# Kernel optimization log

Hardware: AMD Instinct MI355X
Metric: run time of the kernel (lower is better)

## Reference

```python
import jax, jax.numpy as jnp
import numpy as np

HIDDEN = 1024
INTER = 1408
N_EXPERTS = 8
TOP_K = 2
BATCH, SEQ = 2, 1024


def setup_inputs() -> dict:
    key = jax.random.key(0)
    k1, k2, k3, k4, k5 = jax.random.split(key, 5)
    scale_in = 1.0 / np.sqrt(HIDDEN)
    scale_mid = 1.0 / np.sqrt(INTER)
    return {
        "hidden_states": jax.random.normal(k1, (BATCH, SEQ, HIDDEN), dtype=jnp.float32),
        # router: torch Linear(hidden, n_experts, bias=False) -> weight [E, hidden]
        "router_w": jax.random.normal(k2, (N_EXPERTS, HIDDEN), dtype=jnp.float32) * scale_in,
        # per-expert SwiGLU MLP weights, stored pre-transposed for x @ W
        "wg": jax.random.normal(k3, (N_EXPERTS, HIDDEN, INTER), dtype=jnp.float32) * scale_in,
        "wu": jax.random.normal(k4, (N_EXPERTS, HIDDEN, INTER), dtype=jnp.float32) * scale_in,
        "wd": jax.random.normal(k5, (N_EXPERTS, INTER, HIDDEN), dtype=jnp.float32) * scale_mid,
    }


def reference(hidden_states, router_w, wg, wu, wd):
    B, S, D = hidden_states.shape
    x = hidden_states.reshape(-1, D)  # [T, D]
    T = x.shape[0]
    E = router_w.shape[0]

    # Router: softmax over experts in float32, then top-k and renormalize (norm_topk_prob=True)
    logits = x @ router_w.T  # [T, E]
    probs = jax.nn.softmax(logits.astype(jnp.float32), axis=-1)
    topk_w, topk_idx = jax.lax.top_k(probs, TOP_K)  # [T, K]
    topk_w = topk_w / jnp.sum(topk_w, axis=-1, keepdims=True)
    topk_w = topk_w.astype(x.dtype)

    # Dense combine weights [T, E]: zero for unrouted experts -> math-identical to sparse dispatch
    combine = jnp.zeros((T, E), dtype=x.dtype).at[
        jnp.arange(T)[:, None], topk_idx
    ].add(topk_w)

    # Expert SwiGLU MLPs computed as batched GEMMs over experts
    g = jnp.einsum('td,edf->etf', x, wg)  # [E, T, INTER]
    u = jnp.einsum('td,edf->etf', x, wu)
    h = jax.nn.silu(g) * u
    y = jnp.einsum('etf,efd->etd', h, wd)  # [E, T, D]

    out = jnp.einsum('etd,te->td', y, combine)  # weighted combine
    return out.reshape(B, S, D)
```

## Files before the change

kernel.cpp:

```cpp
#include <hip/hip_runtime.h>
#include <math.h>

#define HIDDEN 1024
#define INTER  1408
#define NEXP   8
#define NTOK   2048
#define KSPLIT_LEN 704

typedef short s16x8 __attribute__((ext_vector_type(8)));
typedef float f32x4 __attribute__((ext_vector_type(4)));

static __device__ __forceinline__ short f2b(float f) {
  union { float f; unsigned u; } v; v.f = f;
  unsigned u = v.u;
  unsigned r = (u + 0x7FFFu + ((u >> 16) & 1u)) >> 16;
  return (short)r;
}

__global__ __launch_bounds__(256) void router_choice(
    const float* __restrict__ x, const float* __restrict__ rw,
    int* __restrict__ ce, float2* __restrict__ cw)
{
  int wave = threadIdx.x >> 6;
  int lane = threadIdx.x & 63;
  int t = blockIdx.x * 4 + wave;
  if (t >= NTOK) return;
  const float* xt = x + (size_t)t * HIDDEN;
  float xr[16];
#pragma unroll
  for (int i = 0; i < 16; ++i) xr[i] = xt[lane + 64 * i];
  float logits[NEXP];
#pragma unroll
  for (int e = 0; e < NEXP; ++e) {
    const float* w = rw + e * HIDDEN;
    float acc = 0.f;
#pragma unroll
    for (int i = 0; i < 16; ++i) acc = fmaf(xr[i], w[lane + 64 * i], acc);
#pragma unroll
    for (int off = 32; off > 0; off >>= 1) acc += __shfl_xor(acc, off);
    logits[e] = acc;
  }
  if (lane == 0) {
    float mx = logits[0];
#pragma unroll
    for (int e = 1; e < NEXP; ++e) mx = fmaxf(mx, logits[e]);
    float p[NEXP];
#pragma unroll
    for (int e = 0; e < NEXP; ++e) p[e] = expf(logits[e] - mx);
    int i0 = 0;
#pragma unroll
    for (int e = 1; e < NEXP; ++e) if (p[e] > p[i0]) i0 = e;
    int i1 = (i0 == 0) ? 1 : 0;
#pragma unroll
    for (int e = 0; e < NEXP; ++e) { if (e != i0 && p[e] > p[i1]) i1 = e; }
    float denom = p[i0] + p[i1];
    ce[t] = i0 | (i1 << 8);
    cw[t] = make_float2(p[i0] / denom, p[i1] / denom);
  }
}

__global__ __launch_bounds__(256) void build_lists(
    const int* __restrict__ ce, const float2* __restrict__ cw,
    int* __restrict__ counts, int* __restrict__ base,
    int* __restrict__ tok_list, float* __restrict__ w_list)
{
  int e = blockIdx.x;
  int tid = threadIdx.x;
  __shared__ int hall[256][8];
  __shared__ int hsum[8];
  __shared__ int scan[256];

  int cloc[8];
  int h[8] = {0,0,0,0,0,0,0,0};
  int myc = 0;
#pragma unroll
  for (int j = 0; j < 8; ++j) {
    int c = ce[tid * 8 + j];
    cloc[j] = c;
    int e0 = c & 255, e1 = (c >> 8) & 255;
    h[e0]++; h[e1]++;
    myc += (e0 == e) + (e1 == e);
  }
#pragma unroll
  for (int k = 0; k < 8; ++k) hall[tid][k] = h[k];
  scan[tid] = myc;
  __syncthreads();

  if (tid < 8) {
    int s = 0;
    for (int i = 0; i < 256; ++i) s += hall[i][tid];
    hsum[tid] = s;
  }
  int v = myc;
  for (int off = 1; off < 256; off <<= 1) {
    int prev = (tid >= off) ? scan[tid - off] : 0;
    __syncthreads();
    v = v + prev;
    scan[tid] = v;
    __syncthreads();
  }
  int pos = v - myc;

  if (tid == 0) {
    int b = 0;
    for (int k = 0; k < e; ++k) b += hsum[k];
    base[e] = b;
    counts[e] = hsum[e];
  }

#pragma unroll
  for (int j = 0; j < 8; ++j) {
    int t = tid * 8 + j;
    int c = cloc[j];
    int e0 = c & 255, e1 = (c >> 8) & 255;
    if (e0 == e) {
      float2 w = cw[t];
      tok_list[e * NTOK + pos] = t;
      w_list[e * NTOK + pos] = w.x;
      pos++;
    } else if (e1 == e) {
      float2 w = cw[t];
      tok_list[e * NTOK + pos] = t | (1 << 16);
      w_list[e * NTOK + pos] = w.y;
      pos++;
    }
  }
}

static __device__ __forceinline__ void tconv_tile(
    const float* __restrict__ ie, short* __restrict__ oe,
    int K, int N, int k0, int n0, int tid, float (*t)[65])
{
  int c4 = (tid & 15) * 4, r = tid >> 4;
#pragma unroll
  for (int p = 0; p < 4; ++p) {
    float4 v = *(const float4*)(ie + (size_t)(k0 + r + p * 16) * N + n0 + c4);
    t[r + p * 16][c4 + 0] = v.x;
    t[r + p * 16][c4 + 1] = v.y;
    t[r + p * 16][c4 + 2] = v.z;
    t[r + p * 16][c4 + 3] = v.w;
  }
  __syncthreads();
  int rn = tid >> 2, ck = (tid & 3) * 16;
  s16x8 o0, o1;
#pragma unroll
  for (int j = 0; j < 8; ++j) o0[j] = f2b(t[ck + j][rn]);
#pragma unroll
  for (int j = 0; j < 8; ++j) o1[j] = f2b(t[ck + 8 + j][rn]);
  short* op = oe + (size_t)(n0 + rn) * K + k0 + ck;
  *(s16x8*)(op) = o0;
  *(s16x8*)(op + 8) = o1;
}

__global__ __launch_bounds__(256) void prep_kernel(
    const float* __restrict__ x, const float* __restrict__ wg,
    const float* __restrict__ wu, const float* __restrict__ wd,
    short* __restrict__ xb, short* __restrict__ wgT,
    short* __restrict__ wuT, short* __restrict__ wdT)
{
  __shared__ float t[64][65];
  int id = blockIdx.x;
  int tid = threadIdx.x;
  if (id < 1024) {
    size_t i = (size_t)id * 256 + tid;
    const float4* p = (const float4*)x;
    float4 a = p[2 * i], b = p[2 * i + 1];
    s16x8 o;
    o[0] = f2b(a.x); o[1] = f2b(a.y); o[2] = f2b(a.z); o[3] = f2b(a.w);
    o[4] = f2b(b.x); o[5] = f2b(b.y); o[6] = f2b(b.z); o[7] = f2b(b.w);
    *(s16x8*)(xb + 8 * i) = o;
    return;
  }
  int id2 = id - 1024;
  int seg = id2 / 2816;
  int r = id2 - seg * 2816;
  int e = r / 352;
  int rem = r - e * 352;
  if (seg < 2) {
    int kt = rem / 22, nt = rem - kt * 22;
    const float* ie = (seg == 0 ? wg : wu) + (size_t)e * HIDDEN * INTER;
    short* oe = (seg == 0 ? wgT : wuT) + (size_t)e * HIDDEN * INTER;
    tconv_tile(ie, oe, HIDDEN, INTER, kt * 64, nt * 64, tid, t);
  } else {
    int kt = rem >> 4, nt = rem & 15;
    const float* ie = wd + (size_t)e * HIDDEN * INTER;
    short* oe = wdT + (size_t)e * HIDDEN * INTER;
    tconv_tile(ie, oe, INTER, HIDDEN, kt * 64, nt * 64, tid, t);
  }
}


__global__ __launch_bounds__(256, 2) void gateup_mfma(
    const short* __restrict__ xb, const short* __restrict__ wgT,
    const short* __restrict__ wuT,
    const int* __restrict__ counts, const int* __restrict__ base,
    const int* __restrict__ tok_list, short* __restrict__ hbuf)
{
  int id = blockIdx.x;
  int xcd = id & 7;
  int rest = id >> 3;
  int mslot = rest & 15;
  int g = (rest >> 4) * 8 + xcd;
  int e = g / 11;
  int n0 = (g - e * 11) * 128;
  int cnt = counts[e];
  int m0 = mslot * 128;
  if (m0 >= cnt) return;

  __shared__ short As[128 * 32];
  __shared__ short Bg[128 * 32];
  __shared__ short Bu[128 * 32];
  __shared__ int toks[128];

  int tid = threadIdx.x;
  if (tid < 128) {
    int r = m0 + tid;
    toks[tid] = tok_list[e * NTOK + (r < cnt ? r : cnt - 1)] & 0xFFFF;
  }
  __syncthreads();

  int sr = tid >> 1;
  int h = tid & 1;
  int key = (sr >> 1) & 3;
  int pair = ((2 * h) ^ key) >> 1;
  int sw = (key & 1) * 8;
  const short* gA = xb + (size_t)toks[sr] * HIDDEN + pair * 16;
  const short* gG = wgT + ((size_t)e * INTER + n0 + sr) * HIDDEN + pair * 16;
  const short* gU = wuT + ((size_t)e * INTER + n0 + sr) * HIDDEN + pair * 16;
  short* wA0 = &As[sr * 32 + h * 16 + sw];
  short* wA1 = &As[sr * 32 + h * 16 + (8 - sw)];
  short* wG0 = &Bg[sr * 32 + h * 16 + sw];
  short* wG1 = &Bg[sr * 32 + h * 16 + (8 - sw)];
  short* wU0 = &Bu[sr * 32 + h * 16 + sw];
  short* wU1 = &Bu[sr * 32 + h * 16 + (8 - sw)];

  int wv = tid >> 6, lane = tid & 63;
  int wm = wv & 1, wn = wv >> 1;
  int q = lane >> 4, ml = lane & 15;
  int chk = q ^ ((ml >> 1) & 3);
  const short* ard = &As[(wm * 64 + ml) * 32 + chk * 8];
  const short* grd = &Bg[(wn * 64 + ml) * 32 + chk * 8];
  const short* urd = &Bu[(wn * 64 + ml) * 32 + chk * 8];

  f32x4 accg[4][4], accu[4][4];
#pragma unroll
  for (int i = 0; i < 4; ++i)
#pragma unroll
    for (int j = 0; j < 4; ++j) { accg[i][j] = (f32x4)0.f; accu[i][j] = (f32x4)0.f; }

  s16x8 a0 = *(const s16x8*)(gA);     s16x8 a1 = *(const s16x8*)(gA + 8);
  s16x8 g0 = *(const s16x8*)(gG);     s16x8 g1 = *(const s16x8*)(gG + 8);
  s16x8 u0 = *(const s16x8*)(gU);     s16x8 u1 = *(const s16x8*)(gU + 8);

  for (int k0 = 0; k0 < HIDDEN; k0 += 32) {
    __syncthreads();
    *(s16x8*)wA0 = a0; *(s16x8*)wA1 = a1;
    *(s16x8*)wG0 = g0; *(s16x8*)wG1 = g1;
    *(s16x8*)wU0 = u0; *(s16x8*)wU1 = u1;
    __syncthreads();

    int kn = (k0 + 32) & (HIDDEN - 1);
    a0 = *(const s16x8*)(gA + kn);     a1 = *(const s16x8*)(gA + kn + 8);
    g0 = *(const s16x8*)(gG + kn);     g1 = *(const s16x8*)(gG + kn + 8);
    u0 = *(const s16x8*)(gU + kn);     u1 = *(const s16x8*)(gU + kn + 8);

    s16x8 af[4], gf[4], uf[4];
#pragma unroll
    for (int i = 0; i < 4; ++i) af[i] = *(const s16x8*)(ard + i * 16 * 32);
#pragma unroll
    for (int j = 0; j < 4; ++j) {
      gf[j] = *(const s16x8*)(grd + j * 16 * 32);
      uf[j] = *(const s16x8*)(urd + j * 16 * 32);
    }
#pragma unroll
    for (int i = 0; i < 4; ++i)
#pragma unroll
      for (int j = 0; j < 4; ++j) {
        accg[i][j] = __builtin_amdgcn_mfma_f32_16x16x32_bf16(af[i], gf[j], accg[i][j], 0, 0, 0);
        accu[i][j] = __builtin_amdgcn_mfma_f32_16x16x32_bf16(af[i], uf[j], accu[i][j], 0, 0, 0);
      }
  }

  int hb = base[e];
#pragma unroll
  for (int i = 0; i < 4; ++i)
#pragma unroll
    for (int ii = 0; ii < 4; ++ii) {
      int r = m0 + wm * 64 + i * 16 + q * 4 + ii;
      if (r < cnt) {
        short* hp = hbuf + (size_t)(hb + r) * INTER + n0 + wn * 64 + ml;
#pragma unroll
        for (int j = 0; j < 4; ++j) {
          float gg = accg[i][j][ii], uu = accu[i][j][ii];
          float hh = (gg / (1.f + __expf(-gg))) * uu;
          hp[j * 16] = f2b(hh);
        }
      }
    }
}

__global__ __launch_bounds__(256, 3) void down_mfma(
    const short* __restrict__ hbuf, const short* __restrict__ wdT,
    const int* __restrict__ counts, const int* __restrict__ base,
    const int* __restrict__ tok_list, const float* __restrict__ w_list,
    float* __restrict__ ybuf)
{
  int id = blockIdx.x;
  int xcd = id & 7;
  int rest = id >> 3;
  int mslot = rest & 15;
  int g = (rest >> 4) * 8 + xcd;
  int e = g >> 4;
  int ks = (g >> 3) & 1;
  int n0 = (g & 7) * 128;
  int cnt = counts[e];
  int m0 = mslot * 128;
  if (m0 >= cnt) return;

  __shared__ short As[128 * 32];
  __shared__ short Bs[128 * 32];

  int tid = threadIdx.x;
  int hb = base[e];
  int kbeg = ks * KSPLIT_LEN, kend = kbeg + KSPLIT_LEN;

  int sr = tid >> 1;
  int h = tid & 1;
  int key = (sr >> 1) & 3;
  int pair = ((2 * h) ^ key) >> 1;
  int sw = (key & 1) * 8;
  int ra = m0 + sr; if (ra >= cnt) ra = cnt - 1;
  const short* gA = hbuf + (size_t)(hb + ra) * INTER + pair * 16;
  const short* gB = wdT + ((size_t)e * HIDDEN + n0 + sr) * INTER + pair * 16;
  short* wA0 = &As[sr * 32 + h * 16 + sw];
  short* wA1 = &As[sr * 32 + h * 16 + (8 - sw)];
  short* wB0 = &Bs[sr * 32 + h * 16 + sw];
  short* wB1 = &Bs[sr * 32 + h * 16 + (8 - sw)];

  int wv = tid >> 6, lane = tid & 63;
  int wm = wv & 1, wn = wv >> 1;
  int q = lane >> 4, ml = lane & 15;
  int chk = q ^ ((ml >> 1) & 3);
  const short* ard = &As[(wm * 64 + ml) * 32 + chk * 8];
  const short* brd = &Bs[(wn * 64 + ml) * 32 + chk * 8];

  f32x4 acc[4][4];
#pragma unroll
  for (int i = 0; i < 4; ++i)
#pragma unroll
    for (int j = 0; j < 4; ++j) acc[i][j] = (f32x4)0.f;

  s16x8 a0 = *(const s16x8*)(gA + kbeg);  s16x8 a1 = *(const s16x8*)(gA + kbeg + 8);
  s16x8 b0 = *(const s16x8*)(gB + kbeg);  s16x8 b1 = *(const s16x8*)(gB + kbeg + 8);

  for (int k0 = kbeg; k0 < kend; k0 += 32) {
    __syncthreads();
    *(s16x8*)wA0 = a0; *(s16x8*)wA1 = a1;
    *(s16x8*)wB0 = b0; *(s16x8*)wB1 = b1;
    __syncthreads();

    int kn = k0 + 32; if (kn >= kend) kn = kbeg;
    a0 = *(const s16x8*)(gA + kn);  a1 = *(const s16x8*)(gA + kn + 8);
    b0 = *(const s16x8*)(gB + kn);  b1 = *(const s16x8*)(gB + kn + 8);

    s16x8 af[4], bf[4];
#pragma unroll
    for (int i = 0; i < 4; ++i) af[i] = *(const s16x8*)(ard + i * 16 * 32);
#pragma unroll
    for (int j = 0; j < 4; ++j) bf[j] = *(const s16x8*)(brd + j * 16 * 32);
#pragma unroll
    for (int i = 0; i < 4; ++i)
#pragma unroll
      for (int j = 0; j < 4; ++j)
        acc[i][j] = __builtin_amdgcn_mfma_f32_16x16x32_bf16(af[i], bf[j], acc[i][j], 0, 0, 0);
  }

#pragma unroll
  for (int i = 0; i < 4; ++i)
#pragma unroll
    for (int ii = 0; ii < 4; ++ii) {
      int r = m0 + wm * 64 + i * 16 + q * 4 + ii;
      if (r < cnt) {
        int ent = tok_list[e * NTOK + r];
        int tok = ent & 0xFFFF, slot = ent >> 16;
        float wgt = w_list[e * NTOK + r];
        float* yp = ybuf + ((size_t)(slot * 2 + ks) * NTOK + tok) * HIDDEN
                    + n0 + wn * 64 + ml;
#pragma unroll
        for (int j = 0; j < 4; ++j)
          yp[j * 16] = acc[i][j][ii] * wgt;
      }
    }
}

__global__ __launch_bounds__(256) void combine_kernel(
    const float* __restrict__ ybuf, float* __restrict__ out)
{
  size_t i = (size_t)blockIdx.x * 256 + threadIdx.x;
  const size_t S = (size_t)NTOK * HIDDEN / 4;
  float4 a = ((const float4*)ybuf)[i];
  float4 b = ((const float4*)ybuf)[i + S];
  float4 c = ((const float4*)ybuf)[i + 2 * S];
  float4 d = ((const float4*)ybuf)[i + 3 * S];
  float4 o;
  o.x = (a.x + b.x) + (c.x + d.x);
  o.y = (a.y + b.y) + (c.y + d.y);
  o.z = (a.z + b.z) + (c.z + d.z);
  o.w = (a.w + b.w) + (c.w + d.w);
  ((float4*)out)[i] = o;
}

extern "C" void kernel_launch(void* const* d_in, const int* in_sizes, int n_in,
                              void* d_out, int out_size, void* d_ws, size_t ws_size,
                              hipStream_t stream)
{
  const float* x  = (const float*)d_in[0];
  const float* rw = (const float*)d_in[1];
  const float* wg = (const float*)d_in[2];
  const float* wu = (const float*)d_in[3];
  const float* wd = (const float*)d_in[4];
  float* out = (float*)d_out;

  char* ws = (char*)d_ws;
  int*    counts   = (int*)(ws);
  int*    base     = (int*)(ws + 32);
  int*    tok_list = (int*)(ws + 64);
  float*  w_list   = (float*)(ws + 64 + NEXP * NTOK * 4);
  size_t off = 64 + 2 * (size_t)NEXP * NTOK * 4;
  int*    ce = (int*)(ws + off);     off += NTOK * 4;
  float2* cw = (float2*)(ws + off);  off += NTOK * 8;
  short* xb  = (short*)(ws + off);  off += (size_t)NTOK * HIDDEN * 2;
  short* wgT = (short*)(ws + off);  off += (size_t)NEXP * HIDDEN * INTER * 2;
  short* wuT = (short*)(ws + off);  off += (size_t)NEXP * HIDDEN * INTER * 2;
  short* wdT = (short*)(ws + off);  off += (size_t)NEXP * HIDDEN * INTER * 2;
  short* hbuf = (short*)(ws + off);
  float* ybuf = (float*)wgT;

  router_choice<<<NTOK / 4, 256, 0, stream>>>(x, rw, ce, cw);
  build_lists<<<NEXP, 256, 0, stream>>>(ce, cw, counts, base, tok_list, w_list);

  prep_kernel<<<1024 + 3 * 2816, 256, 0, stream>>>(x, wg, wu, wd, xb, wgT, wuT, wdT);

  gateup_mfma<<<8 * 16 * 11, 256, 0, stream>>>(xb, wgT, wuT, counts, base, tok_list, hbuf);
  down_mfma<<<8 * 16 * 16, 256, 0, stream>>>(hbuf, wdT, counts, base, tok_list, w_list, ybuf);

  combine_kernel<<<(NTOK * HIDDEN / 4) / 256, 256, 0, stream>>>(ybuf, out);
}
```

Measured before the change: 276.9 us.

## Fuse router into prep kernel and transpose weights via registers without LDS

Merges the router/top-k computation into the weight-conversion prep kernel as extra blocks, removing one launch and letting routing overlap the bf16 conversion. The weight transpose now has each thread load 32 strided floats along K straight into registers and write four 16-byte bf16 chunks, with 128-column tiles, instead of staging 64x64 tiles through shared memory with a barrier. Reads stay coalesced across threads along N, but each thread issues many scalar loads with large strides. This may lower memory-level efficiency compared with the float4 loads used before.

```diff
diff --git a/kernel.cpp b/kernel.cpp
--- a/kernel.cpp
+++ b/kernel.cpp
@@ -17,46 +17,112 @@
   return (short)r;
 }
 
-__global__ __launch_bounds__(256) void router_choice(
+__global__ __launch_bounds__(256) void prep_kernel(
     const float* __restrict__ x, const float* __restrict__ rw,
-    int* __restrict__ ce, float2* __restrict__ cw)
-{
-  int wave = threadIdx.x >> 6;
-  int lane = threadIdx.x & 63;
-  int t = blockIdx.x * 4 + wave;
-  if (t >= NTOK) return;
-  const float* xt = x + (size_t)t * HIDDEN;
-  float xr[16];
-#pragma unroll
-  for (int i = 0; i < 16; ++i) xr[i] = xt[lane + 64 * i];
-  float logits[NEXP];
-#pragma unroll
-  for (int e = 0; e < NEXP; ++e) {
-    const float* w = rw + e * HIDDEN;
-    float acc = 0.f;
-#pragma unroll
-    for (int i = 0; i < 16; ++i) acc = fmaf(xr[i], w[lane + 64 * i], acc);
-#pragma unroll
-    for (int off = 32; off > 0; off >>= 1) acc += __shfl_xor(acc, off);
-    logits[e] = acc;
-  }
-  if (lane == 0) {
-    float mx = logits[0];
-#pragma unroll
-    for (int e = 1; e < NEXP; ++e) mx = fmaxf(mx, logits[e]);
-    float p[NEXP];
-#pragma unroll
-    for (int e = 0; e < NEXP; ++e) p[e] = expf(logits[e] - mx);
-    int i0 = 0;
-#pragma unroll
-    for (int e = 1; e < NEXP; ++e) if (p[e] > p[i0]) i0 = e;
-    int i1 = (i0 == 0) ? 1 : 0;
-#pragma unroll
-    for (int e = 0; e < NEXP; ++e) { if (e != i0 && p[e] > p[i1]) i1 = e; }
-    float denom = p[i0] + p[i1];
-    ce[t] = i0 | (i1 << 8);
-    cw[t] = make_float2(p[i0] / denom, p[i1] / denom);
-  }
+    const float* __restrict__ wg, const float* __restrict__ wu,
+    const float* __restrict__ wd,
+    int* __restrict__ ce, float2* __restrict__ cw,
+    short* __restrict__ xb, short* __restrict__ wgT,
+    short* __restrict__ wuT, short* __restrict__ wdT)
+{
+  int id = blockIdx.x;
+  int tid = threadIdx.x;
+
+  if (id < 512) {
+    int wave = tid >> 6;
+    int lane = tid & 63;
+    int t = id * 4 + wave;
+    const float* xt = x + (size_t)t * HIDDEN;
+    float xr[16];
+#pragma unroll
+    for (int i = 0; i < 16; ++i) xr[i] = xt[lane + 64 * i];
+    float logits[NEXP];
+#pragma unroll
+    for (int e = 0; e < NEXP; ++e) {
+      const float* w = rw + e * HIDDEN;
+      float acc = 0.f;
+#pragma unroll
+      for (int i = 0; i < 16; ++i) acc = fmaf(xr[i], w[lane + 64 * i], acc);
+#pragma unroll
+      for (int off = 32; off > 0; off >>= 1) acc += __shfl_xor(acc, off);
+      logits[e] = acc;
+    }
+    if (lane == 0) {
+      float mx = logits[0];
+#pragma unroll
+      for (int e = 1; e < NEXP; ++e) mx = fmaxf(mx, logits[e]);
+      float p[NEXP];
+#pragma unroll
+      for (int e = 0; e < NEXP; ++e) p[e] = expf(logits[e] - mx);
+      int i0 = 0;
+#pragma unroll
+      for (int e = 1; e < NEXP; ++e) if (p[e] > p[i0]) i0 = e;
+      int i1 = (i0 == 0) ? 1 : 0;
+#pragma unroll
+      for (int e = 0; e < NEXP; ++e) { if (e != i0 && p[e] > p[i1]) i1 = e; }
+      float denom = p[i0] + p[i1];
+      ce[t] = i0 | (i1 << 8);
+      cw[t] = make_float2(p[i0] / denom, p[i1] / denom);
+    }
+    return;
+  }
+  id -= 512;
+
+  if (id < 1024) {
+    size_t i = (size_t)id * 256 + tid;
+    const float4* p = (const float4*)x;
+    float4 a = p[2 * i], b = p[2 * i + 1];
+    s16x8 o;
+    o[0] = f2b(a.x); o[1] = f2b(a.y); o[2] = f2b(a.z); o[3] = f2b(a.w);
+    o[4] = f2b(b.x); o[5] = f2b(b.y); o[6] = f2b(b.z); o[7] = f2b(b.w);
+    *(s16x8*)(xb + 8 * i) = o;
+    return;
+  }
+  id -= 1024;
+
+  int seg = id / 1408;
+  int r = id - seg * 1408;
+  int e = r / 176;
+  int rem = r - e * 176;
+  int K, N;
+  const float* ie;
+  short* oe;
+  if (seg < 2) {
+    K = HIDDEN; N = INTER;
+    ie = (seg == 0 ? wg : wu) + (size_t)e * HIDDEN * INTER;
+    oe = (seg == 0 ? wgT : wuT) + (size_t)e * HIDDEN * INTER;
+  } else {
+    K = INTER; N = HIDDEN;
+    ie = wd + (size_t)e * HIDDEN * INTER;
+    oe = wdT + (size_t)e * HIDDEN * INTER;
+  }
+  int ntiles = N >> 7;
+  int kt = rem / ntiles, nt = rem - kt * ntiles;
+  int k0 = kt * 64, n0 = nt * 128;
+
+  int n = n0 + (tid >> 1);
+  int kh = (tid & 1) * 32;
+  const float* ip = ie + (size_t)(k0 + kh) * N + n;
+
+  float v[32];
+#pragma unroll
+  for (int j = 0; j < 32; ++j) v[j] = ip[(size_t)j * N];
+
+  s16x8 o0, o1, o2, o3;
+#pragma unroll
+  for (int j = 0; j < 8; ++j) o0[j] = f2b(v[j]);
+#pragma unroll
+  for (int j = 0; j < 8; ++j) o1[j] = f2b(v[8 + j]);
+#pragma unroll
+  for (int j = 0; j < 8; ++j) o2[j] = f2b(v[16 + j]);
+#pragma unroll
+  for (int j = 0; j < 8; ++j) o3[j] = f2b(v[24 + j]);
+
+  short* op = oe + (size_t)n * K + k0 + kh;
+  *(s16x8*)(op)      = o0;
+  *(s16x8*)(op + 8)  = o1;
+  *(s16x8*)(op + 16) = o2;
+  *(s16x8*)(op + 24) = o3;
 }
 
 __global__ __launch_bounds__(256) void build_lists(
@@ -127,68 +193,6 @@
   }
 }
 
-static __device__ __forceinline__ void tconv_tile(
-    const float* __restrict__ ie, short* __restrict__ oe,
-    int K, int N, int k0, int n0, int tid, float (*t)[65])
-{
-  int c4 = (tid & 15) * 4, r = tid >> 4;
-#pragma unroll
-  for (int p = 0; p < 4; ++p) {
-    float4 v = *(const float4*)(ie + (size_t)(k0 + r + p * 16) * N + n0 + c4);
-    t[r + p * 16][c4 + 0] = v.x;
-    t[r + p * 16][c4 + 1] = v.y;
-    t[r + p * 16][c4 + 2] = v.z;
-    t[r + p * 16][c4 + 3] = v.w;
-  }
-  __syncthreads();
-  int rn = tid >> 2, ck = (tid & 3) * 16;
-  s16x8 o0, o1;
-#pragma unroll
-  for (int j = 0; j < 8; ++j) o0[j] = f2b(t[ck + j][rn]);
-#pragma unroll
-  for (int j = 0; j < 8; ++j) o1[j] = f2b(t[ck + 8 + j][rn]);
-  short* op = oe + (size_t)(n0 + rn) * K + k0 + ck;
-  *(s16x8*)(op) = o0;
-  *(s16x8*)(op + 8) = o1;
-}
-
-__global__ __launch_bounds__(256) void prep_kernel(
-    const float* __restrict__ x, const float* __restrict__ wg,
-    const float* __restrict__ wu, const float* __restrict__ wd,
-    short* __restrict__ xb, short* __restrict__ wgT,
-    short* __restrict__ wuT, short* __restrict__ wdT)
-{
-  __shared__ float t[64][65];
-  int id = blockIdx.x;
-  int tid = threadIdx.x;
-  if (id < 1024) {
-    size_t i = (size_t)id * 256 + tid;
-    const float4* p = (const float4*)x;
-    float4 a = p[2 * i], b = p[2 * i + 1];
-    s16x8 o;
-    o[0] = f2b(a.x); o[1] = f2b(a.y); o[2] = f2b(a.z); o[3] = f2b(a.w);
-    o[4] = f2b(b.x); o[5] = f2b(b.y); o[6] = f2b(b.z); o[7] = f2b(b.w);
-    *(s16x8*)(xb + 8 * i) = o;
-    return;
-  }
-  int id2 = id - 1024;
-  int seg = id2 / 2816;
-  int r = id2 - seg * 2816;
-  int e = r / 352;
-  int rem = r - e * 352;
-  if (seg < 2) {
-    int kt = rem / 22, nt = rem - kt * 22;
-    const float* ie = (seg == 0 ? wg : wu) + (size_t)e * HIDDEN * INTER;
-    short* oe = (seg == 0 ? wgT : wuT) + (size_t)e * HIDDEN * INTER;
-    tconv_tile(ie, oe, HIDDEN, INTER, kt * 64, nt * 64, tid, t);
-  } else {
-    int kt = rem >> 4, nt = rem & 15;
-    const float* ie = wd + (size_t)e * HIDDEN * INTER;
-    short* oe = wdT + (size_t)e * HIDDEN * INTER;
-    tconv_tile(ie, oe, INTER, HIDDEN, kt * 64, nt * 64, tid, t);
-  }
-}
-
 
 __global__ __launch_bounds__(256, 2) void gateup_mfma(
     const short* __restrict__ xb, const short* __restrict__ wgT,
@@ -436,10 +440,9 @@
   short* hbuf = (short*)(ws + off);
   float* ybuf = (float*)wgT;
 
-  router_choice<<<NTOK / 4, 256, 0, stream>>>(x, rw, ce, cw);
+  prep_kernel<<<512 + 1024 + 3 * 1408, 256, 0, stream>>>(
+      x, rw, wg, wu, wd, ce, cw, xb, wgT, wuT, wdT);
   build_lists<<<NEXP, 256, 0, stream>>>(ce, cw, counts, base, tok_list, w_list);
-
-  prep_kernel<<<1024 + 3 * 2816, 256, 0, stream>>>(x, wg, wu, wd, xb, wgT, wuT, wdT);
 
   gateup_mfma<<<8 * 16 * 11, 256, 0, stream>>>(xb, wgT, wuT, counts, base, tok_list, hbuf);
   down_mfma<<<8 * 16 * 16, 256, 0, stream>>>(hbuf, wdT, counts, base, tok_list, w_list, ybuf);
```

After: 287.7 us. +3.9%, slower.
